# Kernel tuning notes

Measured on AMD Instinct MI355X. Metric: run time of the kernel, lower is better.

Reference implementation:

```python
import jax, jax.numpy as jnp
import numpy as np

N_NODES = 100000
N_EDGES = 1600000
NFEAT = 128
NHID = 128
NS = 64
NCLASS = 16
B = 8192


def setup_inputs() -> dict:
    key = jax.random.key(0)
    ks = jax.random.split(key, 12)
    s = jax.random.normal(ks[0], (B, NS), dtype=jnp.float32)
    x = jax.random.normal(ks[1], (N_NODES, NFEAT), dtype=jnp.float32)
    row = jax.random.randint(ks[2], (N_EDGES,), 0, N_NODES)
    col = jax.random.randint(ks[3], (N_EDGES,), 0, N_NODES)
    val = jax.random.uniform(ks[4], (N_EDGES,), dtype=jnp.float32)
    index = jax.random.randint(ks[5], (B,), 0, N_NODES)
    # learned parameters (glorot-ish scale)
    W1 = jax.random.normal(ks[6], (NFEAT, NHID), dtype=jnp.float32) / np.sqrt(NFEAT)
    b1 = jnp.zeros((NHID,), dtype=jnp.float32)
    W2 = jax.random.normal(ks[7], (NHID, NHID), dtype=jnp.float32) / np.sqrt(NHID)
    b2 = jnp.zeros((NHID,), dtype=jnp.float32)
    Wl = jax.random.normal(ks[8], (NHID + NS, NCLASS), dtype=jnp.float32) / np.sqrt(NHID + NS)
    bl = jnp.zeros((NCLASS,), dtype=jnp.float32)
    return {"s": s, "x": x, "row": row, "col": col, "val": val,
            "index": index, "W1": W1, "b1": b1, "W2": W2, "b2": b2,
            "Wl": Wl, "bl": bl}


def reference(s, x, row, col, val, index, W1, b1, W2, b2, Wl, bl):
    n = x.shape[0]

    def spmm(h):
        # adj @ h with adj in COO form: out[r] += val_e * h[c]
        return jax.ops.segment_sum(val[:, None] * h[col], row, num_segments=n)

    # dropout is identity in eval mode (training=False)
    h = jax.nn.relu(spmm(x @ W1) + b1)          # gc1 + relu
    h = spmm(h @ W2) + b2                        # gc2
    z = jnp.concatenate([h[index], s], axis=1) @ Wl + bl  # [B, nclass]
    return jax.nn.log_softmax(z, axis=1)
```

## Files before the change

kernel.cpp:

```cpp
#include <hip/hip_runtime.h>
#include <hip/hip_fp16.h>
#include <math.h>

#define N_NODES 100000
#define N_EDGES 1600000
#define NFEAT 128
#define NHID 128
#define NS 64
#define NCLASS 16
#define BB 8192

#define B1_SHIFT 11
#define NB1 49
#define SUB_SHIFT 5
#define NSUB 3125
#define CHUNKA 2048
#define HWG 256
#define BINC_CAP 2048

typedef unsigned long long ull;
typedef unsigned int uint;


__device__ __forceinline__ unsigned short f2bf(float f) {
  unsigned int u = __float_as_uint(f);
  return (unsigned short)((u + 0x7fffu + ((u >> 16) & 1u)) >> 16);
}
__device__ __forceinline__ unsigned int packbf2(float lo, float hi) {
  return (unsigned int)f2bf(lo) | ((unsigned int)f2bf(hi) << 16);
}


__device__ __forceinline__ __half2 h2zero() {
  return __builtin_bit_cast(__half2, 0u);
}
__device__ __forceinline__ __half2 h2shfl_add(__half2 a, int m) {
  int t = __shfl_xor(__builtin_bit_cast(int, a), m);
  return __hadd2(a, __builtin_bit_cast(__half2, t));
}
__device__ __forceinline__ uint relu2(uint u) {
  uint mm = ((u >> 15) & 0x10001u) * 0xFFFFu;
  return u & ~mm;
}
union U4H { uint4 u4; __half2 h[4]; };

__device__ __forceinline__ void fma_row_h(__half2* acc, __half2 v, uint4 u) {
  U4H q; q.u4 = u;
#pragma unroll
  for (int k = 0; k < 4; ++k) acc[k] = __hfma2(v, q.h[k], acc[k]);
}
__device__ __forceinline__ __half2 edge_vh2(uint e) {
  uint hb = e >> 17;
  return __builtin_bit_cast(__half2, hb * 0x10001u);
}


__device__ __forceinline__ ull pack_edge(float v, int r, int c) {
  return ((ull)(__float_as_uint(v) >> 2) << 34) | ((ull)(unsigned)r << 17) | (unsigned)c;
}
__device__ __forceinline__ int edge_col(ull p) { return (int)(p & 0x1FFFFu); }
__device__ __forceinline__ int edge_row(ull p) { return (int)((unsigned)(p >> 17) & 0x1FFFFu); }
__device__ __forceinline__ float edge_val(ull p) {
  return __uint_as_float(((unsigned)(p >> 34)) << 2);
}
__device__ __forceinline__ uint pack4(ull p) {
  uint hb = (uint)__half_as_ushort(__float2half(edge_val(p)));
  return (uint)edge_col(p) | (hb << 17);
}
__device__ __forceinline__ int keep_test(const uint* keep, int r) {
  return (keep[r >> 5] >> (r & 31)) & 1u;
}


__global__ __launch_bounds__(256) void selbuild_kernel(const int* __restrict__ index,
                                                       int* __restrict__ sel,
                                                       uint* __restrict__ keep) {
  int t = blockIdx.x * 256 + threadIdx.x;
  int r = index[t];
  sel[r] = 1;
  atomicOr(&keep[r >> 5], 1u << (r & 31));
}

__global__ __launch_bounds__(256) void selflag_kernel(const int* __restrict__ row,
                                                      const int* __restrict__ col,
                                                      const int* __restrict__ sel,
                                                      uint* __restrict__ keep) {
  int i = blockIdx.x * blockDim.x + threadIdx.x;
  int stride = gridDim.x * blockDim.x;
  for (; i < N_EDGES; i += stride)
    if (sel[row[i]]) {
      int c = col[i];
      atomicOr(&keep[c >> 5], 1u << (c & 31));
    }
}


__global__ __launch_bounds__(256) void histsub_kernel(const int* __restrict__ row,
                                                      const uint* __restrict__ keep,
                                                      int* __restrict__ subcnt) {
  __shared__ int lh[NSUB];
  int tid = threadIdx.x;
  for (int i = tid; i < NSUB; i += 256) lh[i] = 0;
  __syncthreads();
  for (long i = (long)blockIdx.x * 256 + tid; i < N_EDGES; i += (long)HWG * 256) {
    int r = row[i];
    if (keep_test(keep, r)) atomicAdd(&lh[r >> SUB_SHIFT], 1);
  }
  __syncthreads();
  for (int i = tid; i < NSUB; i += 256) {
    int c = lh[i];
    if (c) atomicAdd(&subcnt[i], c);
  }
}


__global__ __launch_bounds__(1024) void scanall_kernel(const int* __restrict__ subcnt,
                                                       int* __restrict__ sub_offs,
                                                       int* __restrict__ gcur1,
                                                       int* __restrict__ gcur2) {
  __shared__ int sd[1024];
  int tid = threadIdx.x;
  int b0 = tid * 4;
  int vv[4];
  int loc = 0;
#pragma unroll
  for (int k = 0; k < 4; ++k) {
    int i = b0 + k;
    vv[k] = (i < NSUB) ? subcnt[i] : 0;
    loc += vv[k];
  }
  sd[tid] = loc;
  __syncthreads();
  for (int o = 1; o < 1024; o <<= 1) {
    int add = (tid >= o) ? sd[tid - o] : 0;
    __syncthreads();
    sd[tid] += add;
    __syncthreads();
  }
  int pre = sd[tid] - loc;
#pragma unroll
  for (int k = 0; k < 4; ++k) {
    int i = b0 + k;
    if (i < NSUB) {
      sub_offs[i] = pre;
      gcur2[i] = pre;
      if ((i & 63) == 0) gcur1[i >> 6] = pre;
      pre += vv[k];
    }
  }
  if (tid == 1023) sub_offs[NSUB] = sd[1023];
}


__global__ __launch_bounds__(256) void binA_kernel(const int* __restrict__ row,
                                                   const int* __restrict__ col,
                                                   const float* __restrict__ val,
                                                   const uint* __restrict__ keep,
                                                   int* __restrict__ gcur1,
                                                   ull* __restrict__ ebuf1) {
  __shared__ ull stage[CHUNKA];
  __shared__ short bkt[CHUNKA];
  __shared__ int hist[NB1], lofs[NB1 + 1], lcur[NB1], gbase[NB1];
  int tid = threadIdx.x;
  for (long base = (long)blockIdx.x * CHUNKA; base < N_EDGES; base += (long)gridDim.x * CHUNKA) {
    int cnt = (int)min((long)CHUNKA, (long)N_EDGES - base);
    if (tid < NB1) hist[tid] = 0;
    __syncthreads();
    ull e[8]; int bk[8];
#pragma unroll
    for (int v = 0; v < 8; ++v) {
      int i = v * 256 + tid;
      bk[v] = -1;
      if (i < cnt) {
        long g = base + i;
        int r = row[g];
        if (keep_test(keep, r)) {
          e[v] = pack_edge(val[g], r, col[g]);
          bk[v] = r >> B1_SHIFT;
          atomicAdd(&hist[bk[v]], 1);
        }
      }
    }
    __syncthreads();
    if (tid < 64) {
      int h = (tid < NB1) ? hist[tid] : 0;
      int x = h;
      for (int o = 1; o < 64; o <<= 1) {
        int y = __shfl_up(x, o);
        if (tid >= o) x += y;
      }
      if (tid < NB1) { lofs[tid] = x - h; lcur[tid] = x - h; }
      if (tid == 63) lofs[NB1] = x;
    }
    __syncthreads();
#pragma unroll
    for (int v = 0; v < 8; ++v) {
      if (bk[v] >= 0) {
        int pos = atomicAdd(&lcur[bk[v]], 1);
        stage[pos] = e[v];
        bkt[pos] = (short)bk[v];
      }
    }
    __syncthreads();
    if (tid < NB1) {
      int h = hist[tid];
      if (h > 0) gbase[tid] = atomicAdd(&gcur1[tid], h);
    }
    __syncthreads();
    int tot = lofs[NB1];
    for (int s = tid; s < tot; s += 256) {
      int lo = bkt[s];
      ebuf1[gbase[lo] + (s - lofs[lo])] = stage[s];
    }
    __syncthreads();
  }
}


__global__ __launch_bounds__(256) void binB_kernel(const ull* __restrict__ ebuf1,
                                                   const int* __restrict__ sub_offs,
                                                   int* __restrict__ gcur2,
                                                   ull* __restrict__ edat8) {
  __shared__ ull stage[CHUNKA];
  __shared__ short bkt[CHUNKA];
  __shared__ int hist[64], lofs[65], lcur[64], gbase[64];
  int tid = threadIdx.x;
  int b1 = blockIdx.x >> 3, w = blockIdx.x & 7;
  int rbeg = sub_offs[b1 << 6];
  int rend = sub_offs[min((b1 + 1) << 6, NSUB)];
  for (int base = rbeg + w * CHUNKA; base < rend; base += 8 * CHUNKA) {
    int cnt = min(CHUNKA, rend - base);
    if (tid < 64) hist[tid] = 0;
    __syncthreads();
    ull e[8]; int bk[8];
#pragma unroll
    for (int v = 0; v < 8; ++v) {
      int i = v * 256 + tid;
      bk[v] = -1;
      if (i < cnt) {
        e[v] = ebuf1[base + i];
        bk[v] = (edge_row(e[v]) >> SUB_SHIFT) - (b1 << 6);
        atomicAdd(&hist[bk[v]], 1);
      }
    }
    __syncthreads();
    if (tid < 64) {
      int h = hist[tid];
      int x = h;
      for (int o = 1; o < 64; o <<= 1) {
        int y = __shfl_up(x, o);
        if (tid >= o) x += y;
      }
      lofs[tid] = x - h;
      lcur[tid] = x - h;
      if (tid == 63) lofs[64] = x;
    }
    __syncthreads();
#pragma unroll
    for (int v = 0; v < 8; ++v) {
      if (bk[v] >= 0) {
        int pos = atomicAdd(&lcur[bk[v]], 1);
        stage[pos] = e[v];
        bkt[pos] = (short)bk[v];
      }
    }
    __syncthreads();
    if (tid < 64) {
      int h = hist[tid];
      if (h > 0) gbase[tid] = atomicAdd(&gcur2[(b1 << 6) + tid], h);
    }
    __syncthreads();
    for (int s = tid; s < cnt; s += 256) {
      int lo = bkt[s];
      edat8[gbase[lo] + (s - lofs[lo])] = stage[s];
    }
    __syncthreads();
  }
}


__global__ __launch_bounds__(256) void binC_kernel(const int* __restrict__ sub_offs,
                                                   const ull* __restrict__ edat8,
                                                   ull* __restrict__ ebuf1,
                                                   uint* __restrict__ edat4,
                                                   int* __restrict__ offs) {
  __shared__ ull es[BINC_CAP];
  __shared__ int rcnt[32], rcur[32];
  int s = blockIdx.x, tid = threadIdx.x;
  int r0 = s << SUB_SHIFT;
  int beg = sub_offs[s], end = sub_offs[s + 1];
  int n = end - beg;
  if (tid < 32) rcnt[tid] = 0;
  __syncthreads();
  if (n <= BINC_CAP) {
    for (int i = tid; i < n; i += 256) {
      ull p = edat8[beg + i];
      es[i] = p;
      atomicAdd(&rcnt[edge_row(p) & 31], 1);
    }
    __syncthreads();
    if (tid < 32) {
      int h = rcnt[tid];
      int x = h;
      for (int o = 1; o < 32; o <<= 1) {
        int y = __shfl_up(x, o, 32);
        if (tid >= o) x += y;
      }
      rcur[tid] = x - h;
      offs[r0 + tid] = beg + x - h;
      if (s == NSUB - 1 && tid == 31) offs[N_NODES] = end;
    }
    __syncthreads();
    for (int i = tid; i < n; i += 256) {
      ull p = es[i];
      int pos = atomicAdd(&rcur[edge_row(p) & 31], 1);
      edat4[beg + pos] = pack4(p);
    }
  } else {
    for (int i = tid; i < n; i += 256) {
      ull p = edat8[beg + i];
      ebuf1[beg + i] = p;
      atomicAdd(&rcnt[edge_row(p) & 31], 1);
    }
    __syncthreads();
    if (tid < 32) {
      int h = rcnt[tid];
      int x = h;
      for (int o = 1; o < 32; o <<= 1) {
        int y = __shfl_up(x, o, 32);
        if (tid >= o) x += y;
      }
      rcur[tid] = x - h;
      offs[r0 + tid] = beg + x - h;
      if (s == NSUB - 1 && tid == 31) offs[N_NODES] = end;
    }
    __syncthreads();
    for (int i = tid; i < n; i += 256) {
      ull p = ebuf1[beg + i];
      int pos = atomicAdd(&rcur[edge_row(p) & 31], 1);
      edat4[beg + pos] = pack4(p);
    }
  }
}


typedef __attribute__((ext_vector_type(8))) __bf16 bf16x8;
typedef __attribute__((ext_vector_type(4))) float f32x4;
union FragU { uint4 u; bf16x8 b; };

#define LDSTR 68

__global__ __launch_bounds__(256) void gemm1_kernel(const float* __restrict__ A,
                                                    const float* __restrict__ W,
                                                    unsigned short* __restrict__ C,
                                                    int nrows) {
  __shared__ uint As_s[64 * LDSTR];
  __shared__ uint Wt_s[128 * LDSTR];
  int tid = threadIdx.x;

  {
    int n = tid & 127, hh = tid >> 7;
#pragma unroll
    for (int kk = 0; kk < 32; ++kk) {
      int kc = hh * 32 + kk;
      Wt_s[n * LDSTR + kc] = packbf2(W[(2 * kc) * 128 + n], W[(2 * kc + 1) * 128 + n]);
    }
  }

  int w = tid >> 6, lane = tid & 63;
  int quad = lane >> 4, lr = lane & 15;
  int n0 = w * 32;

#pragma unroll
  for (int t = 0; t < 2; ++t) {
    int rbase = blockIdx.x * 128 + t * 64;
    __syncthreads();
    {
      const float4* src = (const float4*)(A + (long)rbase * 128);
#pragma unroll
      for (int i = 0; i < 8; ++i) {
        int f = i * 256 + tid;
        int m = f >> 5;
        float4 v = (rbase + m < nrows) ? src[f] : make_float4(0.f, 0.f, 0.f, 0.f);
        int c = (f & 31) * 2;
        As_s[m * LDSTR + c]     = packbf2(v.x, v.y);
        As_s[m * LDSTR + c + 1] = packbf2(v.z, v.w);
      }
    }
    __syncthreads();

    f32x4 acc[4][2];
#pragma unroll
    for (int mt = 0; mt < 4; ++mt)
#pragma unroll
      for (int nt = 0; nt < 2; ++nt) acc[mt][nt] = (f32x4){0.f, 0.f, 0.f, 0.f};

#pragma unroll
    for (int kk = 0; kk < 4; ++kk) {
      int kc = kk * 16 + quad * 4;
      FragU fb0, fb1;
      fb0.u = *(const uint4*)&Wt_s[(n0 + lr) * LDSTR + kc];
      fb1.u = *(const uint4*)&Wt_s[(n0 + 16 + lr) * LDSTR + kc];
#pragma unroll
      for (int mt = 0; mt < 4; ++mt) {
        FragU fa;
        fa.u = *(const uint4*)&As_s[(mt * 16 + lr) * LDSTR + kc];
        acc[mt][0] = __builtin_amdgcn_mfma_f32_16x16x32_bf16(fa.b, fb0.b, acc[mt][0], 0, 0, 0);
        acc[mt][1] = __builtin_amdgcn_mfma_f32_16x16x32_bf16(fa.b, fb1.b, acc[mt][1], 0, 0, 0);
      }
    }

    __half* cs = (__half*)C;
#pragma unroll
    for (int mt = 0; mt < 4; ++mt) {
#pragma unroll
      for (int nt = 0; nt < 2; ++nt) {
        int col = n0 + nt * 16 + lr;
#pragma unroll
        for (int r = 0; r < 4; ++r) {
          int row = rbase + mt * 16 + quad * 4 + r;
          if (row < nrows) cs[(size_t)row * 128 + col] = __float2half(acc[mt][nt][r]);
        }
      }
    }
  }
}


__global__ __launch_bounds__(256) void gemm2f_kernel(const float* __restrict__ g2,
                                                     const float* __restrict__ W2,
                                                     const float* __restrict__ b2,
                                                     const float* __restrict__ s_in,
                                                     const float* __restrict__ Wl,
                                                     const float* __restrict__ bl,
                                                     float* __restrict__ out) {
  __shared__ uint smem[13056];
  uint* Wt_s = smem;
  uint* As_s = smem + 128 * LDSTR;
  float* ts  = (float*)smem;
  float* Wls = (float*)(smem + 128 * LDSTR);
  int tid = threadIdx.x;
  int rbase = blockIdx.x * 64;

  {
    int n = tid & 127, hh = tid >> 7;
#pragma unroll
    for (int kk = 0; kk < 32; ++kk) {
      int kc = hh * 32 + kk;
      Wt_s[n * LDSTR + kc] = packbf2(W2[(2 * kc) * 128 + n], W2[(2 * kc + 1) * 128 + n]);
    }
  }
  {
    const float4* src = (const float4*)(g2 + (long)rbase * 128);
#pragma unroll
    for (int i = 0; i < 8; ++i) {
      int f = i * 256 + tid;
      int m = f >> 5, c = (f & 31) * 2;
      float4 v = src[f];
      As_s[m * LDSTR + c]     = packbf2(v.x, v.y);
      As_s[m * LDSTR + c + 1] = packbf2(v.z, v.w);
    }
  }
  __syncthreads();

  int w = tid >> 6, lane = tid & 63;
  int quad = lane >> 4, lr = lane & 15;
  int n0 = w * 32;

  f32x4 acc[4][2];
#pragma unroll
  for (int mt = 0; mt < 4; ++mt)
#pragma unroll
    for (int nt = 0; nt < 2; ++nt) acc[mt][nt] = (f32x4){0.f, 0.f, 0.f, 0.f};

#pragma unroll
  for (int kk = 0; kk < 4; ++kk) {
    int kc = kk * 16 + quad * 4;
    FragU fb0, fb1;
    fb0.u = *(const uint4*)&Wt_s[(n0 + lr) * LDSTR + kc];
    fb1.u = *(const uint4*)&Wt_s[(n0 + 16 + lr) * LDSTR + kc];
#pragma unroll
    for (int mt = 0; mt < 4; ++mt) {
      FragU fa;
      fa.u = *(const uint4*)&As_s[(mt * 16 + lr) * LDSTR + kc];
      acc[mt][0] = __builtin_amdgcn_mfma_f32_16x16x32_bf16(fa.b, fb0.b, acc[mt][0], 0, 0, 0);
      acc[mt][1] = __builtin_amdgcn_mfma_f32_16x16x32_bf16(fa.b, fb1.b, acc[mt][1], 0, 0, 0);
    }
  }
  __syncthreads();

#pragma unroll
  for (int mt = 0; mt < 4; ++mt) {
#pragma unroll
    for (int nt = 0; nt < 2; ++nt) {
      int col = n0 + nt * 16 + lr;
      float bv = b2[col];
#pragma unroll
      for (int r = 0; r < 4; ++r)
        ts[(mt * 16 + quad * 4 + r) * 129 + col] = acc[mt][nt][r] + bv;
    }
  }
  for (int i = tid; i < 192 * 16; i += 256) Wls[i] = Wl[i];
  __syncthreads();

  int q = lane & 3;
  int mrow = w * 16 + (lane >> 2);
  int b = rbase + mrow;
  float z[16];
#pragma unroll
  for (int c = 0; c < 16; ++c) z[c] = 0.f;
  int k0 = q * 48;
  for (int kk = 0; kk < 48; ++kk) {
    int k = k0 + kk;
    float xv = (k < 128) ? ts[mrow * 129 + k] : s_in[(long)b * 64 + (k - 128)];
    const float* wp = Wls + k * 16;
#pragma unroll
    for (int c = 0; c < 16; ++c) z[c] = fmaf(xv, wp[c], z[c]);
  }
#pragma unroll
  for (int c = 0; c < 16; ++c) {
    z[c] += __shfl_xor(z[c], 1);
    z[c] += __shfl_xor(z[c], 2);
  }
  if (q == 0) {
#pragma unroll
    for (int c = 0; c < 16; ++c) z[c] += bl[c];
    float mx = z[0];
#pragma unroll
    for (int c = 1; c < 16; ++c) mx = fmaxf(mx, z[c]);
    float sum = 0.f;
#pragma unroll
    for (int c = 0; c < 16; ++c) sum += expf(z[c] - mx);
    float lse = mx + logf(sum);
    float4* ob = (float4*)(out + (long)b * 16);
    ob[0] = make_float4(z[0] - lse, z[1] - lse, z[2] - lse, z[3] - lse);
    ob[1] = make_float4(z[4] - lse, z[5] - lse, z[6] - lse, z[7] - lse);
    ob[2] = make_float4(z[8] - lse, z[9] - lse, z[10] - lse, z[11] - lse);
    ob[3] = make_float4(z[12] - lse, z[13] - lse, z[14] - lse, z[15] - lse);
  }
}


__global__ __launch_bounds__(256) void spmm_row_kernel(const int* __restrict__ offs,
                                                       const uint* __restrict__ edat4,
                                                       const unsigned short* __restrict__ a,
                                                       const float* __restrict__ bias,
                                                       unsigned short* __restrict__ h1,
                                                       const uint* __restrict__ keep) {
  int wave = threadIdx.x >> 6;
  int lane = threadIdx.x & 63;
  int r = blockIdx.x * 4 + wave;
  if (!keep_test(keep, r)) return;
  int g = lane >> 4, l = lane & 15;
  int s = offs[r], e = offs[r + 1];
  __half2 acc[4] = {h2zero(), h2zero(), h2zero(), h2zero()};
  int j = s + g;
  for (; j + 4 < e; j += 8) {
    uint e0 = edat4[j];
    uint e1 = edat4[j + 4];
    uint4 u0 = *(const uint4*)(a + (size_t)(e0 & 0x1FFFFu) * 128 + l * 8);
    uint4 u1 = *(const uint4*)(a + (size_t)(e1 & 0x1FFFFu) * 128 + l * 8);
    fma_row_h(acc, edge_vh2(e0), u0);
    fma_row_h(acc, edge_vh2(e1), u1);
  }
  if (j < e) {
    uint e0 = edat4[j];
    uint4 u = *(const uint4*)(a + (size_t)(e0 & 0x1FFFFu) * 128 + l * 8);
    fma_row_h(acc, edge_vh2(e0), u);
  }
#pragma unroll
  for (int k = 0; k < 4; ++k) {
    acc[k] = h2shfl_add(acc[k], 16);
    acc[k] = h2shfl_add(acc[k], 32);
  }
  if (g == 0) {
    const float* bp = bias + l * 8;
    float4 b0 = *(const float4*)bp;
    float4 b1v = *(const float4*)(bp + 4);
    uint4 o;
    o.x = relu2(__builtin_bit_cast(uint, __hadd2(acc[0], __floats2half2_rn(b0.x, b0.y))));
    o.y = relu2(__builtin_bit_cast(uint, __hadd2(acc[1], __floats2half2_rn(b0.z, b0.w))));
    o.z = relu2(__builtin_bit_cast(uint, __hadd2(acc[2], __floats2half2_rn(b1v.x, b1v.y))));
    o.w = relu2(__builtin_bit_cast(uint, __hadd2(acc[3], __floats2half2_rn(b1v.z, b1v.w))));
    *(uint4*)(h1 + (size_t)r * 128 + l * 8) = o;
  }
}

__global__ __launch_bounds__(256) void spmm_sel_kernel(const int* __restrict__ offs,
                                                       const uint* __restrict__ edat4,
                                                       const unsigned short* __restrict__ h1,
                                                       const int* __restrict__ index,
                                                       float* __restrict__ g2) {
  int wave = threadIdx.x >> 6;
  int lane = threadIdx.x & 63;
  int b = blockIdx.x * 4 + wave;
  int g = lane >> 4, l = lane & 15;
  int r = index[b];
  int s = offs[r], e = offs[r + 1];
  __half2 acc[4] = {h2zero(), h2zero(), h2zero(), h2zero()};
  int j = s + g;
  for (; j + 4 < e; j += 8) {
    uint e0 = edat4[j];
    uint e1 = edat4[j + 4];
    uint4 u0 = *(const uint4*)(h1 + (size_t)(e0 & 0x1FFFFu) * 128 + l * 8);
    uint4 u1 = *(const uint4*)(h1 + (size_t)(e1 & 0x1FFFFu) * 128 + l * 8);
    fma_row_h(acc, edge_vh2(e0), u0);
    fma_row_h(acc, edge_vh2(e1), u1);
  }
  if (j < e) {
    uint e0 = edat4[j];
    uint4 u = *(const uint4*)(h1 + (size_t)(e0 & 0x1FFFFu) * 128 + l * 8);
    fma_row_h(acc, edge_vh2(e0), u);
  }
#pragma unroll
  for (int k = 0; k < 4; ++k) {
    acc[k] = h2shfl_add(acc[k], 16);
    acc[k] = h2shfl_add(acc[k], 32);
  }
  if (g == 0) {
    float* op = g2 + (size_t)b * 128 + l * 8;
    *(float4*)op = make_float4(__low2float(acc[0]), __high2float(acc[0]),
                               __low2float(acc[1]), __high2float(acc[1]));
    *(float4*)(op + 4) = make_float4(__low2float(acc[2]), __high2float(acc[2]),
                                     __low2float(acc[3]), __high2float(acc[3]));
  }
}


extern "C" void kernel_launch(void* const* d_in, const int* in_sizes, int n_in,
                              void* d_out, int out_size, void* d_ws, size_t ws_size,
                              hipStream_t stream) {
  const float* s_in  = (const float*)d_in[0];
  const float* x     = (const float*)d_in[1];
  const int*   row   = (const int*)d_in[2];
  const int*   col   = (const int*)d_in[3];
  const float* val   = (const float*)d_in[4];
  const int*   index = (const int*)d_in[5];
  const float* W1    = (const float*)d_in[6];
  const float* b1    = (const float*)d_in[7];
  const float* W2    = (const float*)d_in[8];
  const float* b2    = (const float*)d_in[9];
  const float* Wl    = (const float*)d_in[10];
  const float* bl    = (const float*)d_in[11];
  float* out = (float*)d_out;

  ull* edat8 = (ull*)d_ws;
  ull* ebuf1 = edat8 + N_EDGES;
  uint* edat4 = (uint*)ebuf1;
  unsigned short* a  = (unsigned short*)(ebuf1 + N_EDGES);
  unsigned short* h1 = a + (size_t)N_NODES * 128;
  float* g2   = (float*)(h1 + (size_t)N_NODES * 128);
  int* sel    = (int*)(g2 + (size_t)BB * 128);
  int* subcnt = sel + N_NODES;
  uint* keep  = (uint*)(subcnt + NSUB);
  int* offs   = (int*)(keep + NSUB);
  int* sub_offs = offs + (N_NODES + 1);
  int* gcur1  = sub_offs + (NSUB + 1);
  int* gcur2  = gcur1 + NB1;

  hipMemsetAsync(sel, 0, (N_NODES + 2 * NSUB) * sizeof(int), stream);

  selbuild_kernel<<<BB / 256, 256, 0, stream>>>(index, sel, keep);
  selflag_kernel<<<4096, 256, 0, stream>>>(row, col, sel, keep);
  histsub_kernel<<<HWG, 256, 0, stream>>>(row, keep, subcnt);
  scanall_kernel<<<1, 1024, 0, stream>>>(subcnt, sub_offs, gcur1, gcur2);

  binA_kernel<<<512, 256, 0, stream>>>(row, col, val, keep, gcur1, ebuf1);
  binB_kernel<<<NB1 * 8, 256, 0, stream>>>(ebuf1, sub_offs, gcur2, edat8);
  binC_kernel<<<NSUB, 256, 0, stream>>>(sub_offs, edat8, ebuf1, edat4, offs);

  gemm1_kernel<<<(N_NODES + 127) / 128, 256, 0, stream>>>(x, W1, a, N_NODES);
  spmm_row_kernel<<<N_NODES / 4, 256, 0, stream>>>(offs, edat4, a, b1, h1, keep);
  spmm_sel_kernel<<<BB / 4, 256, 0, stream>>>(offs, edat4, h1, index, g2);
  gemm2f_kernel<<<BB / 64, 256, 0, stream>>>(g2, W2, b2, s_in, Wl, bl, out);
}
```

Baseline: 296.0 us.

## Compact kept rows into descriptor list and pre-pack bf16 weights once

Adds a kernel that compacts the kept-row bitmask into a dense list of row descriptors (row id, edge start, edge count), so the first SpMM waves index directly into live rows instead of testing the bitmask and reading offsets. Adds a small kernel that converts W1 and W2 to transposed bf16 once, so each GEMM block copies them with vector loads instead of repacking the strided fp32 weights. The SpMM launch still uses a full-size grid, with the surplus waves exiting early on the count check. Two extra launches and a memset are added, and the descriptor list reuses the edat8 buffer.

```diff
diff --git a/kernel.cpp b/kernel.cpp
--- a/kernel.cpp
+++ b/kernel.cpp
@@ -92,6 +92,43 @@
       int c = col[i];
       atomicOr(&keep[c >> 5], 1u << (c & 31));
     }
+}
+
+
+__global__ __launch_bounds__(256) void rdesc_kernel(const uint* __restrict__ keep,
+                                                    const int* __restrict__ offs,
+                                                    ull* __restrict__ rdesc,
+                                                    int* __restrict__ nkept) {
+  int w = blockIdx.x * 256 + threadIdx.x;
+  if (w >= NSUB) return;
+  uint b = keep[w];
+  int c = __popc(b);
+  if (!c) return;
+  int base = atomicAdd(nkept, c);
+  int r0 = w << 5;
+  while (b) {
+    int i = __ffs(b) - 1;
+    int r = r0 + i;
+    int s0 = offs[r], s1 = offs[r + 1];
+    rdesc[base++] = (ull)(uint)r | ((ull)(uint)s0 << 17) | ((ull)(uint)(s1 - s0) << 39);
+    b &= b - 1;
+  }
+}
+
+
+__global__ __launch_bounds__(256) void wprep_kernel(const float* __restrict__ W1,
+                                                    const float* __restrict__ W2,
+                                                    uint* __restrict__ wt1,
+                                                    uint* __restrict__ wt2) {
+  const float* W = blockIdx.x ? W2 : W1;
+  uint* wt = blockIdx.x ? wt2 : wt1;
+  int tid = threadIdx.x;
+  int n = tid & 127, hh = tid >> 7;
+#pragma unroll
+  for (int kk = 0; kk < 32; ++kk) {
+    int kc = hh * 32 + kk;
+    wt[n * 64 + kc] = packbf2(W[(2 * kc) * 128 + n], W[(2 * kc + 1) * 128 + n]);
+  }
 }
 
 
@@ -351,7 +388,7 @@
 #define LDSTR 68
 
 __global__ __launch_bounds__(256) void gemm1_kernel(const float* __restrict__ A,
-                                                    const float* __restrict__ W,
+                                                    const uint* __restrict__ wt1,
                                                     unsigned short* __restrict__ C,
                                                     int nrows) {
   __shared__ uint As_s[64 * LDSTR];
@@ -359,11 +396,11 @@
   int tid = threadIdx.x;
 
   {
-    int n = tid & 127, hh = tid >> 7;
-#pragma unroll
-    for (int kk = 0; kk < 32; ++kk) {
-      int kc = hh * 32 + kk;
-      Wt_s[n * LDSTR + kc] = packbf2(W[(2 * kc) * 128 + n], W[(2 * kc + 1) * 128 + n]);
+    const uint4* src = (const uint4*)wt1;
+#pragma unroll
+    for (int i = 0; i < 8; ++i) {
+      int e = i * 256 + tid;
+      *(uint4*)&Wt_s[(e >> 4) * LDSTR + (e & 15) * 4] = src[e];
     }
   }
 
@@ -428,7 +465,7 @@
 
 
 __global__ __launch_bounds__(256) void gemm2f_kernel(const float* __restrict__ g2,
-                                                     const float* __restrict__ W2,
+                                                     const uint* __restrict__ wt2,
                                                      const float* __restrict__ b2,
                                                      const float* __restrict__ s_in,
                                                      const float* __restrict__ Wl,
@@ -443,11 +480,11 @@
   int rbase = blockIdx.x * 64;
 
   {
-    int n = tid & 127, hh = tid >> 7;
-#pragma unroll
-    for (int kk = 0; kk < 32; ++kk) {
-      int kc = hh * 32 + kk;
-      Wt_s[n * LDSTR + kc] = packbf2(W2[(2 * kc) * 128 + n], W2[(2 * kc + 1) * 128 + n]);
+    const uint4* src = (const uint4*)wt2;
+#pragma unroll
+    for (int i = 0; i < 8; ++i) {
+      int e = i * 256 + tid;
+      *(uint4*)&Wt_s[(e >> 4) * LDSTR + (e & 15) * 4] = src[e];
     }
   }
   {
@@ -541,20 +578,23 @@
 }
 
 
-__global__ __launch_bounds__(256) void spmm_row_kernel(const int* __restrict__ offs,
+__global__ __launch_bounds__(256) void spmm_row_kernel(const ull* __restrict__ rdesc,
                                                        const uint* __restrict__ edat4,
                                                        const unsigned short* __restrict__ a,
                                                        const float* __restrict__ bias,
                                                        unsigned short* __restrict__ h1,
-                                                       const uint* __restrict__ keep) {
+                                                       const int* __restrict__ nkept) {
   int wave = threadIdx.x >> 6;
   int lane = threadIdx.x & 63;
-  int r = blockIdx.x * 4 + wave;
-  if (!keep_test(keep, r)) return;
+  int li = blockIdx.x * 4 + wave;
+  if (li >= *nkept) return;
+  ull d = rdesc[li];
+  int r = (int)(d & 0x1FFFFu);
+  int j0 = (int)((d >> 17) & 0x3FFFFFu);
+  int e = j0 + (int)(d >> 39);
   int g = lane >> 4, l = lane & 15;
-  int s = offs[r], e = offs[r + 1];
   __half2 acc[4] = {h2zero(), h2zero(), h2zero(), h2zero()};
-  int j = s + g;
+  int j = j0 + g;
   for (; j + 4 < e; j += 8) {
     uint e0 = edat4[j];
     uint e1 = edat4[j + 4];
@@ -647,6 +687,7 @@
   ull* edat8 = (ull*)d_ws;
   ull* ebuf1 = edat8 + N_EDGES;
   uint* edat4 = (uint*)ebuf1;
+  ull* rdesc = edat8;
   unsigned short* a  = (unsigned short*)(ebuf1 + N_EDGES);
   unsigned short* h1 = a + (size_t)N_NODES * 128;
   float* g2   = (float*)(h1 + (size_t)N_NODES * 128);
@@ -657,9 +698,14 @@
   int* sub_offs = offs + (N_NODES + 1);
   int* gcur1  = sub_offs + (NSUB + 1);
   int* gcur2  = gcur1 + NB1;
+  int* nkept  = gcur2 + NSUB;
+  uint* wt1   = (uint*)(nkept + 1);
+  uint* wt2   = wt1 + 8192;
 
   hipMemsetAsync(sel, 0, (N_NODES + 2 * NSUB) * sizeof(int), stream);
-
+  hipMemsetAsync(nkept, 0, sizeof(int), stream);
+
+  wprep_kernel<<<2, 256, 0, stream>>>(W1, W2, wt1, wt2);
   selbuild_kernel<<<BB / 256, 256, 0, stream>>>(index, sel, keep);
   selflag_kernel<<<4096, 256, 0, stream>>>(row, col, sel, keep);
   histsub_kernel<<<HWG, 256, 0, stream>>>(row, keep, subcnt);
@@ -669,8 +715,10 @@
   binB_kernel<<<NB1 * 8, 256, 0, stream>>>(ebuf1, sub_offs, gcur2, edat8);
   binC_kernel<<<NSUB, 256, 0, stream>>>(sub_offs, edat8, ebuf1, edat4, offs);
 
-  gemm1_kernel<<<(N_NODES + 127) / 128, 256, 0, stream>>>(x, W1, a, N_NODES);
-  spmm_row_kernel<<<N_NODES / 4, 256, 0, stream>>>(offs, edat4, a, b1, h1, keep);
+  rdesc_kernel<<<(NSUB + 255) / 256, 256, 0, stream>>>(keep, offs, rdesc, nkept);
+
+  gemm1_kernel<<<(N_NODES + 127) / 128, 256, 0, stream>>>(x, wt1, a, N_NODES);
+  spmm_row_kernel<<<N_NODES / 4, 256, 0, stream>>>(rdesc, edat4, a, b1, h1, nkept);
   spmm_sel_kernel<<<BB / 4, 256, 0, stream>>>(offs, edat4, h1, index, g2);
-  gemm2f_kernel<<<BB / 64, 256, 0, stream>>>(g2, W2, b2, s_in, Wl, bl, out);
-}
+  gemm2f_kernel<<<BB / 64, 256, 0, stream>>>(g2, wt2, b2, s_in, Wl, bl, out);
+}
```

New measurement: 309.0 us. +4.4%, slower.
